# Optimization experiments

Hardware: AMD Instinct MI355X
Metric: run time of the kernel (lower is better)

Reference implementation:

```python
import jax, jax.numpy as jnp
import numpy as np

NPOINT = 1024
RADIUS = 0.15
NSAMPLE = 32
BN_EPS = 1e-5


def farthest_point_sample(xyz, npoint):
    # xyz: [B, N, 3] -> idx [B, npoint]
    B, N, _ = xyz.shape

    def step(carry, _):
        dmin, far = carry
        cent = jnp.take_along_axis(xyz, far[:, None, None], axis=1)  # [B,1,3]
        d = jnp.sum((xyz - cent) ** 2, axis=-1)                      # [B,N]
        dmin = jnp.minimum(dmin, d)
        nxt = jnp.argmax(dmin, axis=-1).astype(jnp.int32)
        return (dmin, nxt), far

    init = (jnp.full((B, N), 1e10, xyz.dtype), jnp.zeros((B,), jnp.int32))
    _, idx = jax.lax.scan(step, init, None, length=npoint)
    return idx.T  # [B, npoint]


def ball_query(radius, nsample, xyz, new_xyz):
    # xyz: [B,N,3], new_xyz: [B,S,3] -> idx [B,S,nsample]
    B, S, _ = new_xyz.shape
    N = xyz.shape[1]
    sqr = jnp.sum((new_xyz[:, :, None, :] - xyz[:, None, :, :]) ** 2, axis=-1)  # [B,S,N]
    ar = jnp.broadcast_to(jnp.arange(N, dtype=jnp.int32), (B, S, N))
    gidx = jnp.where(sqr > radius * radius, N, ar)
    gidx = jnp.sort(gidx, axis=-1)[:, :, :nsample]
    first = gidx[:, :, :1]
    return jnp.where(gidx == N, first, gidx)


def setup_inputs() -> dict:
    key = jax.random.key(0)
    ks = jax.random.split(key, 8)
    B, N, Cin, Cmlp, Cout = 8, 4096, 64, 128, 256
    xyz = jax.random.uniform(ks[0], (B, N, 3), dtype=jnp.float32)
    t = jax.random.normal(ks[1], (B, 128), dtype=jnp.float32)
    points = jax.random.normal(ks[2], (B, N, Cin), dtype=jnp.float32)
    W1 = jax.random.normal(ks[3], (Cin, Cmlp), dtype=jnp.float32) / np.sqrt(Cin)
    b1 = jnp.zeros((Cmlp,), jnp.float32)
    Wc = jax.random.normal(ks[4], (Cmlp, Cout), dtype=jnp.float32) / np.sqrt(Cmlp)
    bc = jnp.zeros((Cout,), jnp.float32)
    gamma = jnp.ones((Cout,), jnp.float32)
    beta = jnp.zeros((Cout,), jnp.float32)
    return {"xyz": xyz, "t": t, "points": points, "W1": W1, "b1": b1,
            "Wc": Wc, "bc": bc, "gamma": gamma, "beta": beta}


def reference(xyz, t, points, W1, b1, Wc, bc, gamma, beta):
    # t (time embedding) is unused in the visible (truncated) forward body.
    B, N, _ = xyz.shape
    # 1) farthest point sampling -> centers
    fps_idx = farthest_point_sample(xyz, NPOINT)                     # [B,S]
    new_xyz = jnp.take_along_axis(xyz, fps_idx[:, :, None], axis=1)  # [B,S,3]
    # 2) radius ball-query grouping
    gidx = ball_query(RADIUS, NSAMPLE, xyz, new_xyz)                 # [B,S,ns]
    # 3) pointwise MLP on features, then group (gather)
    feats = points @ W1 + b1                                          # [B,N,Cmlp]
    grouped = jax.vmap(lambda f, i: f[i])(feats, gidx)                # [B,S,ns,Cmlp]
    # 4) GroupConv: 1x1 conv + BatchNorm(train stats) + ReLU
    h = jnp.einsum('bsnc,co->bsno', grouped, Wc) + bc                 # [B,S,ns,Cout]
    mean = jnp.mean(h, axis=(0, 1, 2))
    var = jnp.var(h, axis=(0, 1, 2))
    h = jax.nn.relu((h - mean) / jnp.sqrt(var + BN_EPS) * gamma + beta)
    # 5) max-pool over neighborhood
    new_points = jnp.max(h, axis=2)                                   # [B,S,Cout]
    return new_points
```

## Files before the change

### kernel.cpp

```cpp
#include <hip/hip_runtime.h>
#include <stdint.h>

#define BN 8
#define NPT 4096
#define NS 1024
#define KS 32
#define CIN 64
#define CMID 128
#define COUT 256
#define NGRP (BN*NS)
#define NBINS 512

typedef short bf16x8 __attribute__((ext_vector_type(8)));
typedef float f32x4 __attribute__((ext_vector_type(4)));
typedef unsigned long long u64;

__device__ __forceinline__ float bf2f(unsigned short u){
  union { unsigned int i; float f; } v; v.i = ((unsigned int)u) << 16; return v.f;
}
__device__ __forceinline__ unsigned short f2bf(float f){
  union { float f; unsigned int i; } v; v.f = f;
  unsigned int r = (v.i + 0x7fffu + ((v.i >> 16) & 1u)) >> 16;
  return (unsigned short)r;
}
__device__ __forceinline__ uint32_t pack2(float a, float b){
  return (uint32_t)f2bf(a) | ((uint32_t)f2bf(b) << 16);
}
__device__ __forceinline__ float ldf(const void* p, size_t i, bool isbf){
  return isbf ? bf2f(((const unsigned short*)p)[i]) : ((const float*)p)[i];
}
__device__ __forceinline__ bool detect_bf(const void* gamma){
  return ((const unsigned int*)gamma)[0] == 0x3F803F80u;
}
template<int CTRL>
__device__ __forceinline__ u64 dpp_u64(u64 x){
  int lo = (int)(unsigned int)(x & 0xFFFFFFFFull);
  int hi = (int)(unsigned int)(x >> 32);
  int nlo = __builtin_amdgcn_update_dpp(0, lo, CTRL, 0xF, 0xF, true);
  int nhi = __builtin_amdgcn_update_dpp(0, hi, CTRL, 0xF, 0xF, true);
  return ((u64)(unsigned int)nhi << 32) | (unsigned int)nlo;
}
__device__ __forceinline__ u64 u64max(u64 a, u64 b){ return a > b ? a : b; }
__device__ __forceinline__ u64 wave_max_u64(u64 k){
  k = u64max(k, dpp_u64<0x121>(k));
  k = u64max(k, dpp_u64<0x122>(k));
  k = u64max(k, dpp_u64<0x124>(k));
  k = u64max(k, dpp_u64<0x128>(k));
  k = u64max(k, dpp_u64<0x142>(k));
  k = u64max(k, dpp_u64<0x143>(k));
  return k;
}
__device__ __forceinline__ u64 readlane63_u64(u64 k){
  unsigned lo = (unsigned)__builtin_amdgcn_readlane((int)(unsigned)(k & 0xFFFFFFFFull), 63);
  unsigned hi = (unsigned)__builtin_amdgcn_readlane((int)(unsigned)(k >> 32), 63);
  return ((u64)hi << 32) | lo;
}
__device__ __forceinline__ void bbox6(float x, float y, float z,
                                      float&xl,float&xh,float&yl,float&yh,float&zl,float&zh){
  xl=x; xh=x; yl=y; yh=y; zl=z; zh=z;
  #pragma unroll
  for (int off=1; off<64; off<<=1){
    xl=fminf(xl,__shfl_xor(xl,off,64)); xh=fmaxf(xh,__shfl_xor(xh,off,64));
    yl=fminf(yl,__shfl_xor(yl,off,64)); yh=fmaxf(yh,__shfl_xor(yh,off,64));
    zl=fminf(zl,__shfl_xor(zl,off,64)); zh=fmaxf(zh,__shfl_xor(zh,off,64));
  }
}

__device__ __forceinline__ unsigned mcode(float x, float y, float z){
  int ix = (int)(x*16.f); ix = ix<0?0:(ix>15?15:ix);
  int iy = (int)(y*16.f); iy = iy<0?0:(iy>15?15:iy);
  int iz = (int)(z*8.f);  iz = iz<0?0:(iz>7?7:iz);
  return ((unsigned)(iy&1))      | ((unsigned)(ix&1)<<1) | ((unsigned)(iz&1)<<2)
       | ((unsigned)(iy&2)<<2)   | ((unsigned)(ix&2)<<3) | ((unsigned)(iz&2)<<4)
       | ((unsigned)(iy&4)<<4)   | ((unsigned)(ix&4)<<5) | ((unsigned)(iz&4)<<6)
       | ((unsigned)(iy&8)<<6)   | ((unsigned)(ix&8)<<7);
}

__global__ __launch_bounds__(512, 3)
void k_front(const void* __restrict__ xyz,
             const void* __restrict__ points,
             const void* __restrict__ W1,
             const void* __restrict__ Wc,
             const void* __restrict__ gamma,
             float* __restrict__ newxyz,
             unsigned short* __restrict__ featsb,
             unsigned short* __restrict__ wct,
             float* __restrict__ ps, float* __restrict__ pq, int bigws)
{
  int tid = threadIdx.x;
  int bid = blockIdx.x;
  bool isbf = detect_bf(gamma);
  __shared__ __align__(16) char smem[65536];
  __shared__ unsigned tsum[512];
  __shared__ u64 wk[2][8];

  if (bid < 8){
    float* ssx = (float*)smem;
    float* ssy = ssx + NPT;
    float* ssz = ssy + NPT;
    unsigned short* snl = (unsigned short*)(ssz + NPT);
    unsigned* hist = (unsigned*)(smem + 57344);
    size_t xb = (size_t)bid*NPT*3;
    int base = tid*8;
    for (int i=tid; i<2048; i+=512) hist[i]=0;
    __syncthreads();
    unsigned codes[8];
    #pragma unroll
    for (int k=0;k<8;k++){
      size_t p = xb + (size_t)(base+k)*3;
      unsigned c = mcode(ldf(xyz,p,isbf), ldf(xyz,p+1,isbf), ldf(xyz,p+2,isbf));
      codes[k]=c;
      atomicAdd(&hist[c],1u);
    }
    __syncthreads();
    unsigned l0=hist[tid*4],l1=hist[tid*4+1],l2=hist[tid*4+2],l3=hist[tid*4+3];
    unsigned s = l0+l1+l2+l3;
    tsum[tid]=s; __syncthreads();
    for (int off=1; off<512; off<<=1){
      unsigned v = (tid>=off)? tsum[tid-off]:0u; __syncthreads();
      tsum[tid]+=v; __syncthreads();
    }
    unsigned ex0 = tsum[tid]-s;
    hist[tid*4]=ex0; hist[tid*4+1]=ex0+l0; hist[tid*4+2]=ex0+l0+l1; hist[tid*4+3]=ex0+l0+l1+l2;
    __syncthreads();
    #pragma unroll
    for (int k=0;k<8;k++){
      size_t p = xb + (size_t)(base+k)*3;
      float x=ldf(xyz,p,isbf), y=ldf(xyz,p+1,isbf), z=ldf(xyz,p+2,isbf);
      unsigned pos = atomicAdd(&hist[codes[k]],1u);
      ssx[pos]=x; ssy[pos]=y; ssz[pos]=z; snl[pos]=(unsigned short)(4095-(base+k));
    }
    __syncthreads();
    int lane = tid & 63, wv = tid >> 6;
    float qx0,qx1,qx2,qx3,qx4,qx5,qx6,qx7;
    float qy0,qy1,qy2,qy3,qy4,qy5,qy6,qy7;
    float qz0,qz1,qz2,qz3,qz4,qz5,qz6,qz7;
    float dd0,dd1,dd2,dd3,dd4,dd5,dd6,dd7;
    unsigned lk0,lk1,lk2,lk3,lk4,lk5,lk6,lk7;
#define LOADS(k) { int p = (wv<<9) + ((k)<<6) + lane; \
  qx##k=ssx[p]; qy##k=ssy[p]; qz##k=ssz[p]; dd##k=1e10f; \
  lk##k = ((unsigned)snl[p]<<12) | (unsigned)p; }
    LOADS(0) LOADS(1) LOADS(2) LOADS(3) LOADS(4) LOADS(5) LOADS(6) LOADS(7)
#undef LOADS
    float qbxl=0.f,qbxh=0.f,qbyl=0.f,qbyh=0.f,qbzl=0.f,qbzh=0.f;
    int lq = lane & 7;
#define CB(k) { float xl,xh,yl,yh,zl,zh; bbox6(qx##k,qy##k,qz##k,xl,xh,yl,yh,zl,zh); \
  if (lq==(k)){ qbxl=xl; qbxh=xh; qbyl=yl; qbyh=yh; qbzl=zl; qbzh=zh; } }
    CB(0) CB(1) CB(2) CB(3) CB(4) CB(5) CB(6) CB(7)
#undef CB
    float cx=ldf(xyz,xb,isbf), cy=ldf(xyz,xb+1,isbf), cz=ldf(xyz,xb+2,isbf);
    if (tid==0){ float* o = newxyz + (size_t)bid*NS*3; o[0]=cx; o[1]=cy; o[2]=cz; }
    u64 ckey = ((u64)__float_as_uint(1e10f) << 32);
    for (int it=1; it<NS; ++it){
      int par = it & 1;
      float exd = fmaxf(fmaxf(__fsub_rn(qbxl,cx), __fsub_rn(cx,qbxh)), 0.f);
      float eyd = fmaxf(fmaxf(__fsub_rn(qbyl,cy), __fsub_rn(cy,qbyh)), 0.f);
      float ezd = fmaxf(fmaxf(__fsub_rn(qbzl,cz), __fsub_rn(cz,qbzh)), 0.f);
      float lb2 = exd*exd + eyd*eyd + ezd*ezd;
      float wtmax = __uint_as_float((unsigned)(ckey >> 32));
      unsigned amask = (unsigned)__ballot(lb2*0.999f < wtmax) & 0xFFu;
      if (amask){
#define FPS_STEP(k) if (amask & (1u<<(k))){ \
  float dx=__fsub_rn(qx##k,cx), dy=__fsub_rn(qy##k,cy), dz=__fsub_rn(qz##k,cz); \
  float d=__fadd_rn(__fadd_rn(__fmul_rn(dx,dx),__fmul_rn(dy,dy)),__fmul_rn(dz,dz)); \
  dd##k=fminf(dd##k,d); }
        FPS_STEP(0) FPS_STEP(1) FPS_STEP(2) FPS_STEP(3)
        FPS_STEP(4) FPS_STEP(5) FPS_STEP(6) FPS_STEP(7)
#undef FPS_STEP
#define KEYK(k) ( ((u64)__float_as_uint(dd##k) << 32) | lk##k )
        u64 t0=u64max(KEYK(0),KEYK(1)), t2=u64max(KEYK(2),KEYK(3));
        u64 t4=u64max(KEYK(4),KEYK(5)), t6=u64max(KEYK(6),KEYK(7));
#undef KEYK
        t0=u64max(t0,t2); t4=u64max(t4,t6);
        u64 key = u64max(t0,t4);
        ckey = readlane63_u64(wave_max_u64(key));
      }
      if (lane == 0) wk[par][wv] = ckey;
      __syncthreads();
      const u64* w8 = wk[par];
      u64 k0 = u64max(u64max(u64max(w8[0],w8[1]), u64max(w8[2],w8[3])),
                      u64max(u64max(w8[4],w8[5]), u64max(w8[6],w8[7])));
      unsigned spos = (unsigned)(k0 & 0xFFFu);
      cx = ssx[spos]; cy = ssy[spos]; cz = ssz[spos];
      if (tid==0){ float* o = newxyz + ((size_t)bid*NS + it)*3; o[0]=cx; o[1]=cy; o[2]=cz; }
    }
  } else if (bid == 8){
    for (int i=tid; i<CMID*COUT; i+=512){
      int k = i >> 8, n = i & 255;
      unsigned short w = isbf ? ((const unsigned short*)Wc)[i] : f2bf(((const float*)Wc)[i]);
      wct[(size_t)n*CMID + k] = w;
    }
    if (!bigws){
      for (int i=tid; i<COUT*NBINS; i+=512){ ps[i]=0.f; pq[i]=0.f; }
    }
  } else {
    float* w1s = (float*)smem;
    float* pts = (float*)(smem + 32768);
    int rb = bid - 9;
    int r0g = rb*64;
    for (int i=tid; i<CIN*CMID; i+=512) w1s[i] = ldf(W1, i, isbf);
    for (int i=tid; i<64*CIN; i+=512)   pts[i] = ldf(points, (size_t)r0g*CIN + i, isbf);
    __syncthreads();
    int o0 = (tid & 15) * 8, r0 = (tid >> 4) * 2;
    float acc0[8]={0,0,0,0,0,0,0,0}, acc1[8]={0,0,0,0,0,0,0,0};
    for (int c=0;c<CIN;c++){
      float a0 = pts[r0*CIN + c], a1 = pts[(r0+1)*CIN + c];
      const float* wr = &w1s[c*CMID + o0];
      #pragma unroll
      for (int j=0;j<8;j++){ acc0[j] = fmaf(a0, wr[j], acc0[j]); acc1[j] = fmaf(a1, wr[j], acc1[j]); }
    }
    unsigned short* f0 = featsb + ((size_t)(r0g + r0))*CMID + o0;
    uint4 u;
    u.x=pack2(acc0[0],acc0[1]); u.y=pack2(acc0[2],acc0[3]); u.z=pack2(acc0[4],acc0[5]); u.w=pack2(acc0[6],acc0[7]);
    *(uint4*)f0 = u;
    u.x=pack2(acc1[0],acc1[1]); u.y=pack2(acc1[2],acc1[3]); u.z=pack2(acc1[4],acc1[5]); u.w=pack2(acc1[6],acc1[7]);
    *(uint4*)(f0 + CMID) = u;
  }
}

__global__ __launch_bounds__(256)
void k_ballq(const void* __restrict__ xyz,
             const void* __restrict__ gamma,
             const float* __restrict__ newxyz,
             int* __restrict__ gidx)
{
  __shared__ float sp[NPT*3];
  __shared__ int slots[4][KS];
  int tid = threadIdx.x;
  bool isbf = detect_bf(gamma);
  int cb = blockIdx.x * 64;
  int b = cb >> 10;
  size_t xb = (size_t)b*NPT*3;
  for (int i=tid; i<NPT*3; i+=256) sp[i] = ldf(xyz, xb + i, isbf);
  __syncthreads();
  int lane = tid & 63, wv = tid >> 6;
  const float rr = (float)(0.15*0.15);
  for (int j=0; j<16; ++j){
    int cid = cb + wv*16 + j;
    const float* cc = newxyz + (size_t)cid*3;
    float cx=cc[0], cy=cc[1], cz=cc[2];
    int cnt = 0;
    for (int ch=0; ch<64; ++ch){
      int p = ch*64 + lane;
      float dx=__fsub_rn(sp[p*3],cx), dy=__fsub_rn(sp[p*3+1],cy), dz=__fsub_rn(sp[p*3+2],cz);
      float d=__fadd_rn(__fadd_rn(__fmul_rn(dx,dx),__fmul_rn(dy,dy)),__fmul_rn(dz,dz));
      bool in = !(d > rr);
      u64 mk = __ballot(in);
      int pos = cnt + __popcll(mk & ((1ull<<lane) - 1ull));
      if (in && pos < KS) slots[wv][pos] = p;
      cnt += __popcll(mk);
      if (cnt >= KS) break;
    }
    int total = cnt < KS ? cnt : KS;
    if (lane < KS){
      int v = (lane < total) ? slots[wv][lane] : slots[wv][0];
      gidx[(size_t)cid*KS + lane] = v;
    }
  }
}

__global__ __launch_bounds__(256)
void k_group(const unsigned short* __restrict__ featsb,
             const unsigned short* __restrict__ wct,
             const int* __restrict__ gidx,
             float* __restrict__ ps, float* __restrict__ pq,
             float* __restrict__ hM, int bigws)
{
  int tid = threadIdx.x;
  int bs0 = blockIdx.x * 2;
  __shared__ unsigned short g[2][32][136];
  __shared__ int gi[2][KS];
  if (tid < 2*KS) gi[tid>>5][tid&31] = gidx[(size_t)bs0*KS + tid];
  __syncthreads();
  {
    int r = tid >> 3, sg = tid & 7;
    size_t fb = (size_t)(bs0>>10)*NPT;
    #pragma unroll
    for (int gg=0; gg<2; gg++){
      const unsigned short* src = featsb + (fb + gi[gg][r])*CMID + sg*16;
      uint4 v0 = *(const uint4*)src;
      uint4 v1 = *(const uint4*)(src + 8);
      *(uint4*)(&g[gg][r][sg*16])     = v0;
      *(uint4*)(&g[gg][r][sg*16 + 8]) = v1;
    }
  }
  __syncthreads();
  int lane = tid & 63, wv = tid >> 6;
  int m = lane & 15, quad = lane >> 4;
  f32x4 acc[2][2][4];
  #pragma unroll
  for (int gg=0; gg<2; gg++)
    #pragma unroll
    for (int a=0;a<2;a++)
      #pragma unroll
      for (int b2=0;b2<4;b2++) acc[gg][a][b2] = (f32x4){0.f,0.f,0.f,0.f};
  int n0 = wv * 64;
  #pragma unroll
  for (int k0=0; k0<CMID; k0+=32){
    bf16x8 a00 = *(const bf16x8*)(&g[0][m][k0 + quad*8]);
    bf16x8 a01 = *(const bf16x8*)(&g[0][16 + m][k0 + quad*8]);
    bf16x8 a10 = *(const bf16x8*)(&g[1][m][k0 + quad*8]);
    bf16x8 a11 = *(const bf16x8*)(&g[1][16 + m][k0 + quad*8]);
    #pragma unroll
    for (int nt=0; nt<4; nt++){
      int n = n0 + nt*16 + m;
      bf16x8 bb = *(const bf16x8*)(wct + (size_t)n*CMID + k0 + quad*8);
      acc[0][0][nt] = __builtin_amdgcn_mfma_f32_16x16x32_bf16(a00, bb, acc[0][0][nt], 0, 0, 0);
      acc[0][1][nt] = __builtin_amdgcn_mfma_f32_16x16x32_bf16(a01, bb, acc[0][1][nt], 0, 0, 0);
      acc[1][0][nt] = __builtin_amdgcn_mfma_f32_16x16x32_bf16(a10, bb, acc[1][0][nt], 0, 0, 0);
      acc[1][1][nt] = __builtin_amdgcn_mfma_f32_16x16x32_bf16(a11, bb, acc[1][1][nt], 0, 0, 0);
    }
  }
  #pragma unroll
  for (int gg=0; gg<2; gg++){
    int bs = bs0 + gg;
    #pragma unroll
    for (int nt=0; nt<4; nt++){
      float s=0.f, q=0.f, hx=-3.402823466e38f;
      #pragma unroll
      for (int mt=0; mt<2; mt++)
        #pragma unroll
        for (int rg=0; rg<4; rg++){ float h = acc[gg][mt][nt][rg]; s += h; q += h*h; hx = fmaxf(hx,h); }
      s += __shfl_xor(s,16,64); q += __shfl_xor(q,16,64); hx = fmaxf(hx, __shfl_xor(hx,16,64));
      s += __shfl_xor(s,32,64); q += __shfl_xor(q,32,64); hx = fmaxf(hx, __shfl_xor(hx,32,64));
      if (quad == 0){
        int o = n0 + nt*16 + m;
        if (bigws){
          ps[(size_t)o*NGRP + bs] = s;
          pq[(size_t)o*NGRP + bs] = q;
        } else {
          atomicAdd(&ps[(size_t)o*NBINS + (bs & (NBINS-1))], s);
          atomicAdd(&pq[(size_t)o*NBINS + (bs & (NBINS-1))], q);
        }
        hM[(size_t)bs*COUT + o] = hx;
      }
    }
  }
}

__global__ __launch_bounds__(256)
void k_bnprep(const float* __restrict__ ps, const float* __restrict__ pq,
              const void* __restrict__ gamma, const void* __restrict__ beta,
              float* __restrict__ av, float* __restrict__ cv, int nbins)
{
  int tid = threadIdx.x, o = blockIdx.x;
  bool isbf = detect_bf(gamma);
  float s=0.f, q=0.f;
  for (int i=tid; i<nbins; i+=256){ s += ps[(size_t)o*nbins + i]; q += pq[(size_t)o*nbins + i]; }
  #pragma unroll
  for (int off=1; off<64; off<<=1){ s += __shfl_xor(s,off,64); q += __shfl_xor(q,off,64); }
  __shared__ float ls[4], lq[4];
  int lane = tid & 63, wv = tid >> 6;
  if (lane == 0){ ls[wv]=s; lq[wv]=q; }
  __syncthreads();
  if (tid == 0){
    float S = ls[0]+ls[1]+ls[2]+ls[3], Q = lq[0]+lq[1]+lq[2]+lq[3];
    const float invM = 1.0f/262144.0f;
    float mean = S*invM;
    float var  = fmaxf(Q*invM - mean*mean, 0.f);
    float inv  = 1.0f/sqrtf(var + 1e-5f);
    float a = ldf(gamma,o,isbf)*inv;
    float c = ldf(beta,o,isbf) - mean*a;
    av[o]=a; cv[o]=c;
  }
}

__global__ __launch_bounds__(256)
void k_bnfinal(const float* __restrict__ hM,
               const float* __restrict__ av, const float* __restrict__ cv,
               const void* __restrict__ gamma, void* __restrict__ out)
{
  int idx = blockIdx.x*256 + threadIdx.x;
  int o = idx & 255;
  float v = fmaxf(hM[idx]*av[o] + cv[o], 0.f);
  if (detect_bf(gamma)) ((unsigned short*)out)[idx] = f2bf(v);
  else                  ((float*)out)[idx] = v;
}

extern "C" void kernel_launch(void* const* d_in, const int* in_sizes, int n_in,
                              void* d_out, int out_size, void* d_ws, size_t ws_size,
                              hipStream_t stream)
{
  const void* xyz    = d_in[0];
  const void* points = d_in[2];
  const void* W1     = d_in[3];
  const void* Wc     = d_in[5];
  const void* gamma  = d_in[7];
  const void* beta   = d_in[8];

  char* ws = (char*)d_ws;
  unsigned short* featsb = (unsigned short*)(ws + 0);
  unsigned short* wct    = (unsigned short*)(ws + 8388608);
  float* newxyz          = (float*)(ws + 8454144);
  int*   gidx            = (int*)(ws + 8552448);
  bool bigws = ws_size >= (size_t)34768896;
  float *ps, *pq, *hM, *av, *cv;
  if (bigws){
    ps = (float*)(ws + 9601024);
    pq = (float*)(ws + 17989632);
    hM = (float*)(ws + 26378240);
    av = (float*)(ws + 34766848);
    cv = (float*)(ws + 34767872);
  } else {
    hM = (float*)(ws + 9601024);
    ps = (float*)(ws + 17989632);
    pq = (float*)(ws + 18513920);
    av = (float*)(ws + 19038208);
    cv = (float*)(ws + 19039232);
  }

  hipLaunchKernelGGL(k_front,  dim3(521), dim3(512), 0, stream,
                     xyz, points, W1, Wc, gamma, newxyz, featsb, wct, ps, pq, (int)bigws);
  hipLaunchKernelGGL(k_ballq,  dim3(128), dim3(256), 0, stream, xyz, gamma, newxyz, gidx);
  hipLaunchKernelGGL(k_group,  dim3(4096), dim3(256), 0, stream,
                     featsb, wct, gidx, ps, pq, hM, (int)bigws);
  hipLaunchKernelGGL(k_bnprep, dim3(256),  dim3(256), 0, stream,
                     ps, pq, gamma, beta, av, cv, bigws ? NGRP : NBINS);
  hipLaunchKernelGGL(k_bnfinal,dim3(8192), dim3(256), 0, stream, hM, av, cv, gamma, d_out);
}
```

Before: 955.9 us.

## Run two FPS batches per block sharing one barrier per iteration

The farthest-point-sampling stage now handles two batches per workgroup (4 blocks instead of 8), interleaving both batches' updates so that each iteration needs one barrier for two batches. Point data is repacked into an xyz+index float4 array so each point load is a single vector LDS read. This shortens per-step overhead from barriers and LDS reads but doubles the serial work per block and raises register pressure (launch bounds lowered to 2 blocks). FPS is latency bound, so the serial chain per block gets longer while the barrier cost is amortised.

```diff
diff --git a/kernel.cpp b/kernel.cpp
--- a/kernel.cpp
+++ b/kernel.cpp
@@ -76,7 +76,7 @@
        | ((unsigned)(iy&8)<<6)   | ((unsigned)(ix&8)<<7);
 }
 
-__global__ __launch_bounds__(512, 3)
+__global__ __launch_bounds__(512, 2)
 void k_front(const void* __restrict__ xyz,
              const void* __restrict__ points,
              const void* __restrict__ W1,
@@ -90,101 +90,135 @@
   int tid = threadIdx.x;
   int bid = blockIdx.x;
   bool isbf = detect_bf(gamma);
-  __shared__ __align__(16) char smem[65536];
+  __shared__ __align__(16) float ssp[2][NPT*4];
+  __shared__ unsigned hist[2048];
   __shared__ unsigned tsum[512];
-  __shared__ u64 wk[2][8];
-
-  if (bid < 8){
-    float* ssx = (float*)smem;
-    float* ssy = ssx + NPT;
-    float* ssz = ssy + NPT;
-    unsigned short* snl = (unsigned short*)(ssz + NPT);
-    unsigned* hist = (unsigned*)(smem + 57344);
-    size_t xb = (size_t)bid*NPT*3;
+  __shared__ u64 wk[2][2][8];
+
+  if (bid < 4){
+    int lane = tid & 63, wv = tid >> 6;
     int base = tid*8;
-    for (int i=tid; i<2048; i+=512) hist[i]=0;
-    __syncthreads();
-    unsigned codes[8];
-    #pragma unroll
-    for (int k=0;k<8;k++){
-      size_t p = xb + (size_t)(base+k)*3;
-      unsigned c = mcode(ldf(xyz,p,isbf), ldf(xyz,p+1,isbf), ldf(xyz,p+2,isbf));
-      codes[k]=c;
-      atomicAdd(&hist[c],1u);
-    }
-    __syncthreads();
-    unsigned l0=hist[tid*4],l1=hist[tid*4+1],l2=hist[tid*4+2],l3=hist[tid*4+3];
-    unsigned s = l0+l1+l2+l3;
-    tsum[tid]=s; __syncthreads();
-    for (int off=1; off<512; off<<=1){
-      unsigned v = (tid>=off)? tsum[tid-off]:0u; __syncthreads();
-      tsum[tid]+=v; __syncthreads();
-    }
-    unsigned ex0 = tsum[tid]-s;
-    hist[tid*4]=ex0; hist[tid*4+1]=ex0+l0; hist[tid*4+2]=ex0+l0+l1; hist[tid*4+3]=ex0+l0+l1+l2;
-    __syncthreads();
-    #pragma unroll
-    for (int k=0;k<8;k++){
-      size_t p = xb + (size_t)(base+k)*3;
-      float x=ldf(xyz,p,isbf), y=ldf(xyz,p+1,isbf), z=ldf(xyz,p+2,isbf);
-      unsigned pos = atomicAdd(&hist[codes[k]],1u);
-      ssx[pos]=x; ssy[pos]=y; ssz[pos]=z; snl[pos]=(unsigned short)(4095-(base+k));
-    }
-    __syncthreads();
-    int lane = tid & 63, wv = tid >> 6;
-    float qx0,qx1,qx2,qx3,qx4,qx5,qx6,qx7;
-    float qy0,qy1,qy2,qy3,qy4,qy5,qy6,qy7;
-    float qz0,qz1,qz2,qz3,qz4,qz5,qz6,qz7;
-    float dd0,dd1,dd2,dd3,dd4,dd5,dd6,dd7;
-    unsigned lk0,lk1,lk2,lk3,lk4,lk5,lk6,lk7;
-#define LOADS(k) { int p = (wv<<9) + ((k)<<6) + lane; \
-  qx##k=ssx[p]; qy##k=ssy[p]; qz##k=ssz[p]; dd##k=1e10f; \
-  lk##k = ((unsigned)snl[p]<<12) | (unsigned)p; }
-    LOADS(0) LOADS(1) LOADS(2) LOADS(3) LOADS(4) LOADS(5) LOADS(6) LOADS(7)
+    for (int c=0;c<2;c++){
+      size_t xb = (size_t)(bid*2+c)*NPT*3;
+      float* sp = ssp[c];
+      for (int i=tid; i<2048; i+=512) hist[i]=0;
+      __syncthreads();
+      unsigned codes[8];
+      #pragma unroll
+      for (int k=0;k<8;k++){
+        size_t p = xb + (size_t)(base+k)*3;
+        unsigned cc = mcode(ldf(xyz,p,isbf), ldf(xyz,p+1,isbf), ldf(xyz,p+2,isbf));
+        codes[k]=cc;
+        atomicAdd(&hist[cc],1u);
+      }
+      __syncthreads();
+      unsigned l0=hist[tid*4],l1=hist[tid*4+1],l2=hist[tid*4+2],l3=hist[tid*4+3];
+      unsigned s = l0+l1+l2+l3;
+      tsum[tid]=s; __syncthreads();
+      for (int off=1; off<512; off<<=1){
+        unsigned v = (tid>=off)? tsum[tid-off]:0u; __syncthreads();
+        tsum[tid]+=v; __syncthreads();
+      }
+      unsigned ex0 = tsum[tid]-s;
+      hist[tid*4]=ex0; hist[tid*4+1]=ex0+l0; hist[tid*4+2]=ex0+l0+l1; hist[tid*4+3]=ex0+l0+l1+l2;
+      __syncthreads();
+      #pragma unroll
+      for (int k=0;k<8;k++){
+        size_t p = xb + (size_t)(base+k)*3;
+        float x=ldf(xyz,p,isbf), y=ldf(xyz,p+1,isbf), z=ldf(xyz,p+2,isbf);
+        unsigned pos = atomicAdd(&hist[codes[k]],1u);
+        sp[pos*4]=x; sp[pos*4+1]=y; sp[pos*4+2]=z;
+        ((unsigned*)sp)[pos*4+3] = (unsigned)(4095-(base+k));
+      }
+      __syncthreads();
+    }
+#define DECL(C) \
+    float qx##C##0,qx##C##1,qx##C##2,qx##C##3,qx##C##4,qx##C##5,qx##C##6,qx##C##7; \
+    float qy##C##0,qy##C##1,qy##C##2,qy##C##3,qy##C##4,qy##C##5,qy##C##6,qy##C##7; \
+    float qz##C##0,qz##C##1,qz##C##2,qz##C##3,qz##C##4,qz##C##5,qz##C##6,qz##C##7; \
+    float dd##C##0,dd##C##1,dd##C##2,dd##C##3,dd##C##4,dd##C##5,dd##C##6,dd##C##7; \
+    unsigned lk##C##0,lk##C##1,lk##C##2,lk##C##3,lk##C##4,lk##C##5,lk##C##6,lk##C##7;
+    DECL(A) DECL(B)
+#undef DECL
+#define LOADS(C,S,k) { int p = (wv<<9) + ((k)<<6) + lane; \
+  const f32x4 v = *(const f32x4*)&ssp[S][p*4]; \
+  qx##C##k=v[0]; qy##C##k=v[1]; qz##C##k=v[2]; dd##C##k=1e10f; \
+  lk##C##k = (__float_as_uint(v[3])<<12) | (unsigned)p; }
+    LOADS(A,0,0) LOADS(A,0,1) LOADS(A,0,2) LOADS(A,0,3)
+    LOADS(A,0,4) LOADS(A,0,5) LOADS(A,0,6) LOADS(A,0,7)
+    LOADS(B,1,0) LOADS(B,1,1) LOADS(B,1,2) LOADS(B,1,3)
+    LOADS(B,1,4) LOADS(B,1,5) LOADS(B,1,6) LOADS(B,1,7)
 #undef LOADS
-    float qbxl=0.f,qbxh=0.f,qbyl=0.f,qbyh=0.f,qbzl=0.f,qbzh=0.f;
     int lq = lane & 7;
-#define CB(k) { float xl,xh,yl,yh,zl,zh; bbox6(qx##k,qy##k,qz##k,xl,xh,yl,yh,zl,zh); \
-  if (lq==(k)){ qbxl=xl; qbxh=xh; qbyl=yl; qbyh=yh; qbzl=zl; qbzh=zh; } }
-    CB(0) CB(1) CB(2) CB(3) CB(4) CB(5) CB(6) CB(7)
+#define BDECL(C) float qbxl##C=0.f,qbxh##C=0.f,qbyl##C=0.f,qbyh##C=0.f,qbzl##C=0.f,qbzh##C=0.f;
+    BDECL(A) BDECL(B)
+#undef BDECL
+#define CB(C,k) { float xl,xh,yl,yh,zl,zh; bbox6(qx##C##k,qy##C##k,qz##C##k,xl,xh,yl,yh,zl,zh); \
+  if (lq==(k)){ qbxl##C=xl; qbxh##C=xh; qbyl##C=yl; qbyh##C=yh; qbzl##C=zl; qbzh##C=zh; } }
+    CB(A,0) CB(A,1) CB(A,2) CB(A,3) CB(A,4) CB(A,5) CB(A,6) CB(A,7)
+    CB(B,0) CB(B,1) CB(B,2) CB(B,3) CB(B,4) CB(B,5) CB(B,6) CB(B,7)
 #undef CB
-    float cx=ldf(xyz,xb,isbf), cy=ldf(xyz,xb+1,isbf), cz=ldf(xyz,xb+2,isbf);
-    if (tid==0){ float* o = newxyz + (size_t)bid*NS*3; o[0]=cx; o[1]=cy; o[2]=cz; }
-    u64 ckey = ((u64)__float_as_uint(1e10f) << 32);
+    size_t xbA = (size_t)(bid*2)*NPT*3, xbB = (size_t)(bid*2+1)*NPT*3;
+    float cxA=ldf(xyz,xbA,isbf), cyA=ldf(xyz,xbA+1,isbf), czA=ldf(xyz,xbA+2,isbf);
+    float cxB=ldf(xyz,xbB,isbf), cyB=ldf(xyz,xbB+1,isbf), czB=ldf(xyz,xbB+2,isbf);
+    if (tid==0){
+      float* o = newxyz + (size_t)(bid*2)*NS*3;   o[0]=cxA; o[1]=cyA; o[2]=czA;
+      float* p = newxyz + (size_t)(bid*2+1)*NS*3; p[0]=cxB; p[1]=cyB; p[2]=czB;
+    }
+    u64 ckeyA = ((u64)__float_as_uint(1e10f) << 32);
+    u64 ckeyB = ckeyA;
     for (int it=1; it<NS; ++it){
       int par = it & 1;
-      float exd = fmaxf(fmaxf(__fsub_rn(qbxl,cx), __fsub_rn(cx,qbxh)), 0.f);
-      float eyd = fmaxf(fmaxf(__fsub_rn(qbyl,cy), __fsub_rn(cy,qbyh)), 0.f);
-      float ezd = fmaxf(fmaxf(__fsub_rn(qbzl,cz), __fsub_rn(cz,qbzh)), 0.f);
-      float lb2 = exd*exd + eyd*eyd + ezd*ezd;
-      float wtmax = __uint_as_float((unsigned)(ckey >> 32));
-      unsigned amask = (unsigned)__ballot(lb2*0.999f < wtmax) & 0xFFu;
-      if (amask){
-#define FPS_STEP(k) if (amask & (1u<<(k))){ \
-  float dx=__fsub_rn(qx##k,cx), dy=__fsub_rn(qy##k,cy), dz=__fsub_rn(qz##k,cz); \
-  float d=__fadd_rn(__fadd_rn(__fmul_rn(dx,dx),__fmul_rn(dy,dy)),__fmul_rn(dz,dz)); \
-  dd##k=fminf(dd##k,d); }
-        FPS_STEP(0) FPS_STEP(1) FPS_STEP(2) FPS_STEP(3)
-        FPS_STEP(4) FPS_STEP(5) FPS_STEP(6) FPS_STEP(7)
-#undef FPS_STEP
-#define KEYK(k) ( ((u64)__float_as_uint(dd##k) << 32) | lk##k )
-        u64 t0=u64max(KEYK(0),KEYK(1)), t2=u64max(KEYK(2),KEYK(3));
-        u64 t4=u64max(KEYK(4),KEYK(5)), t6=u64max(KEYK(6),KEYK(7));
-#undef KEYK
-        t0=u64max(t0,t2); t4=u64max(t4,t6);
-        u64 key = u64max(t0,t4);
-        ckey = readlane63_u64(wave_max_u64(key));
-      }
-      if (lane == 0) wk[par][wv] = ckey;
+#define UPDATE(C, CI) { \
+      float exd = fmaxf(fmaxf(__fsub_rn(qbxl##C,cx##C), __fsub_rn(cx##C,qbxh##C)), 0.f); \
+      float eyd = fmaxf(fmaxf(__fsub_rn(qbyl##C,cy##C), __fsub_rn(cy##C,qbyh##C)), 0.f); \
+      float ezd = fmaxf(fmaxf(__fsub_rn(qbzl##C,cz##C), __fsub_rn(cz##C,qbzh##C)), 0.f); \
+      float lb2 = exd*exd + eyd*eyd + ezd*ezd; \
+      float wtmax = __uint_as_float((unsigned)(ckey##C >> 32)); \
+      unsigned amask = (unsigned)__ballot(lb2*0.999f < wtmax) & 0xFFu; \
+      if (amask){ \
+         \
+        if (amask & 1u)  { float dx=__fsub_rn(qx##C##0,cx##C), dy=__fsub_rn(qy##C##0,cy##C), dz=__fsub_rn(qz##C##0,cz##C); \
+          dd##C##0=fminf(dd##C##0,__fadd_rn(__fadd_rn(__fmul_rn(dx,dx),__fmul_rn(dy,dy)),__fmul_rn(dz,dz))); } \
+        if (amask & 2u)  { float dx=__fsub_rn(qx##C##1,cx##C), dy=__fsub_rn(qy##C##1,cy##C), dz=__fsub_rn(qz##C##1,cz##C); \
+          dd##C##1=fminf(dd##C##1,__fadd_rn(__fadd_rn(__fmul_rn(dx,dx),__fmul_rn(dy,dy)),__fmul_rn(dz,dz))); } \
+        if (amask & 4u)  { float dx=__fsub_rn(qx##C##2,cx##C), dy=__fsub_rn(qy##C##2,cy##C), dz=__fsub_rn(qz##C##2,cz##C); \
+          dd##C##2=fminf(dd##C##2,__fadd_rn(__fadd_rn(__fmul_rn(dx,dx),__fmul_rn(dy,dy)),__fmul_rn(dz,dz))); } \
+        if (amask & 8u)  { float dx=__fsub_rn(qx##C##3,cx##C), dy=__fsub_rn(qy##C##3,cy##C), dz=__fsub_rn(qz##C##3,cz##C); \
+          dd##C##3=fminf(dd##C##3,__fadd_rn(__fadd_rn(__fmul_rn(dx,dx),__fmul_rn(dy,dy)),__fmul_rn(dz,dz))); } \
+        if (amask & 16u) { float dx=__fsub_rn(qx##C##4,cx##C), dy=__fsub_rn(qy##C##4,cy##C), dz=__fsub_rn(qz##C##4,cz##C); \
+          dd##C##4=fminf(dd##C##4,__fadd_rn(__fadd_rn(__fmul_rn(dx,dx),__fmul_rn(dy,dy)),__fmul_rn(dz,dz))); } \
+        if (amask & 32u) { float dx=__fsub_rn(qx##C##5,cx##C), dy=__fsub_rn(qy##C##5,cy##C), dz=__fsub_rn(qz##C##5,cz##C); \
+          dd##C##5=fminf(dd##C##5,__fadd_rn(__fadd_rn(__fmul_rn(dx,dx),__fmul_rn(dy,dy)),__fmul_rn(dz,dz))); } \
+        if (amask & 64u) { float dx=__fsub_rn(qx##C##6,cx##C), dy=__fsub_rn(qy##C##6,cy##C), dz=__fsub_rn(qz##C##6,cz##C); \
+          dd##C##6=fminf(dd##C##6,__fadd_rn(__fadd_rn(__fmul_rn(dx,dx),__fmul_rn(dy,dy)),__fmul_rn(dz,dz))); } \
+        if (amask & 128u){ float dx=__fsub_rn(qx##C##7,cx##C), dy=__fsub_rn(qy##C##7,cy##C), dz=__fsub_rn(qz##C##7,cz##C); \
+          dd##C##7=fminf(dd##C##7,__fadd_rn(__fadd_rn(__fmul_rn(dx,dx),__fmul_rn(dy,dy)),__fmul_rn(dz,dz))); } \
+        u64 t0=u64max(((u64)__float_as_uint(dd##C##0)<<32)|lk##C##0, ((u64)__float_as_uint(dd##C##1)<<32)|lk##C##1); \
+        u64 t2=u64max(((u64)__float_as_uint(dd##C##2)<<32)|lk##C##2, ((u64)__float_as_uint(dd##C##3)<<32)|lk##C##3); \
+        u64 t4=u64max(((u64)__float_as_uint(dd##C##4)<<32)|lk##C##4, ((u64)__float_as_uint(dd##C##5)<<32)|lk##C##5); \
+        u64 t6=u64max(((u64)__float_as_uint(dd##C##6)<<32)|lk##C##6, ((u64)__float_as_uint(dd##C##7)<<32)|lk##C##7); \
+        t0=u64max(t0,t2); t4=u64max(t4,t6); \
+        ckey##C = readlane63_u64(wave_max_u64(u64max(t0,t4))); \
+      } \
+      if (lane == 0) wk[CI][par][wv] = ckey##C; }
+      UPDATE(A, 0)
+      UPDATE(B, 1)
+#undef UPDATE
       __syncthreads();
-      const u64* w8 = wk[par];
-      u64 k0 = u64max(u64max(u64max(w8[0],w8[1]), u64max(w8[2],w8[3])),
-                      u64max(u64max(w8[4],w8[5]), u64max(w8[6],w8[7])));
-      unsigned spos = (unsigned)(k0 & 0xFFFu);
-      cx = ssx[spos]; cy = ssy[spos]; cz = ssz[spos];
-      if (tid==0){ float* o = newxyz + ((size_t)bid*NS + it)*3; o[0]=cx; o[1]=cy; o[2]=cz; }
-    }
-  } else if (bid == 8){
+#define FINAL(C, CI, S, BATCH) { \
+      const u64* w8 = wk[CI][par]; \
+      u64 k0 = u64max(u64max(u64max(w8[0],w8[1]), u64max(w8[2],w8[3])), \
+                      u64max(u64max(w8[4],w8[5]), u64max(w8[6],w8[7]))); \
+      unsigned spos = (unsigned)(k0 & 0xFFFu); \
+      const f32x4 v = *(const f32x4*)&ssp[S][spos*4]; \
+      cx##C=v[0]; cy##C=v[1]; cz##C=v[2]; \
+      if (tid==0){ float* o = newxyz + ((size_t)(BATCH)*NS + it)*3; o[0]=cx##C; o[1]=cy##C; o[2]=cz##C; } }
+      FINAL(A, 0, 0, bid*2)
+      FINAL(B, 1, 1, bid*2+1)
+#undef FINAL
+    }
+  } else if (bid == 4){
     for (int i=tid; i<CMID*COUT; i+=512){
       int k = i >> 8, n = i & 255;
       unsigned short w = isbf ? ((const unsigned short*)Wc)[i] : f2bf(((const float*)Wc)[i]);
@@ -194,9 +228,9 @@
       for (int i=tid; i<COUT*NBINS; i+=512){ ps[i]=0.f; pq[i]=0.f; }
     }
   } else {
-    float* w1s = (float*)smem;
-    float* pts = (float*)(smem + 32768);
-    int rb = bid - 9;
+    float* w1s = ssp[0];
+    float* pts = ssp[0] + CIN*CMID;
+    int rb = bid - 5;
     int r0g = rb*64;
     for (int i=tid; i<CIN*CMID; i+=512) w1s[i] = ldf(W1, i, isbf);
     for (int i=tid; i<64*CIN; i+=512)   pts[i] = ldf(points, (size_t)r0g*CIN + i, isbf);
@@ -409,7 +443,7 @@
     cv = (float*)(ws + 19039232);
   }
 
-  hipLaunchKernelGGL(k_front,  dim3(521), dim3(512), 0, stream,
+  hipLaunchKernelGGL(k_front,  dim3(517), dim3(512), 0, stream,
                      xyz, points, W1, Wc, gamma, newxyz, featsb, wct, ps, pq, (int)bigws);
   hipLaunchKernelGGL(k_ballq,  dim3(128), dim3(256), 0, stream, xyz, gamma, newxyz, gidx);
   hipLaunchKernelGGL(k_group,  dim3(4096), dim3(256), 0, stream,
```

Result: slower. 1.426 ms (+49.2%).

## Fuse ball query into group kernel and merge BN prep with final pass

Applied to the files above, without the earlier changes.

The ball-query kernel is folded into the grouping/MFMA kernel. Each block now finds its own two centers' neighbours in shared memory and gathers features directly, so the gidx round trip through global memory and one launch go away. The BN statistics reduction and the normalize/ReLU pass become one kernel, with each block handling one output channel. In exchange, every one of the 4096 blocks reloads the full 48KB per-batch xyz array into shared memory, which also limits occupancy. The fused BN writes use a 256-element stride across threads, so its memory accesses are no longer coalesced.

```diff
diff --git a/kernel.cpp b/kernel.cpp
--- a/kernel.cpp
+++ b/kernel.cpp
@@ -219,26 +219,32 @@
 }
 
 __global__ __launch_bounds__(256)
-void k_ballq(const void* __restrict__ xyz,
-             const void* __restrict__ gamma,
-             const float* __restrict__ newxyz,
-             int* __restrict__ gidx)
+void k_groupq(const void* __restrict__ xyz,
+              const float* __restrict__ newxyz,
+              const unsigned short* __restrict__ featsb,
+              const unsigned short* __restrict__ wct,
+              const void* __restrict__ gamma,
+              float* __restrict__ ps, float* __restrict__ pq,
+              float* __restrict__ hM, int bigws)
 {
-  __shared__ float sp[NPT*3];
-  __shared__ int slots[4][KS];
   int tid = threadIdx.x;
+  int bs0 = blockIdx.x * 2;
+  int b = bs0 >> 10;
   bool isbf = detect_bf(gamma);
-  int cb = blockIdx.x * 64;
-  int b = cb >> 10;
+  __shared__ __align__(16) char smem[49152];
+  __shared__ int gi[2][KS];
+  int lane = tid & 63, wv = tid >> 6;
+
+  float* sp = (float*)smem;
   size_t xb = (size_t)b*NPT*3;
   for (int i=tid; i<NPT*3; i+=256) sp[i] = ldf(xyz, xb + i, isbf);
   __syncthreads();
-  int lane = tid & 63, wv = tid >> 6;
-  const float rr = (float)(0.15*0.15);
-  for (int j=0; j<16; ++j){
-    int cid = cb + wv*16 + j;
+
+  if (wv < 2){
+    int cid = bs0 + wv;
     const float* cc = newxyz + (size_t)cid*3;
     float cx=cc[0], cy=cc[1], cz=cc[2];
+    const float rr = (float)(0.15*0.15);
     int cnt = 0;
     for (int ch=0; ch<64; ++ch){
       int p = ch*64 + lane;
@@ -247,45 +253,35 @@
       bool in = !(d > rr);
       u64 mk = __ballot(in);
       int pos = cnt + __popcll(mk & ((1ull<<lane) - 1ull));
-      if (in && pos < KS) slots[wv][pos] = p;
+      if (in && pos < KS) gi[wv][pos] = p;
       cnt += __popcll(mk);
       if (cnt >= KS) break;
     }
     int total = cnt < KS ? cnt : KS;
     if (lane < KS){
-      int v = (lane < total) ? slots[wv][lane] : slots[wv][0];
-      gidx[(size_t)cid*KS + lane] = v;
-    }
-  }
-}
-
-__global__ __launch_bounds__(256)
-void k_group(const unsigned short* __restrict__ featsb,
-             const unsigned short* __restrict__ wct,
-             const int* __restrict__ gidx,
-             float* __restrict__ ps, float* __restrict__ pq,
-             float* __restrict__ hM, int bigws)
-{
-  int tid = threadIdx.x;
-  int bs0 = blockIdx.x * 2;
-  __shared__ unsigned short g[2][32][136];
-  __shared__ int gi[2][KS];
-  if (tid < 2*KS) gi[tid>>5][tid&31] = gidx[(size_t)bs0*KS + tid];
+      int v = (lane < total) ? gi[wv][lane] : gi[wv][0];
+      gi[wv][lane] = v;
+    }
+  }
   __syncthreads();
+
+  typedef unsigned short grow_t[32][136];
+  grow_t* g = (grow_t*)smem;
   {
     int r = tid >> 3, sg = tid & 7;
-    size_t fb = (size_t)(bs0>>10)*NPT;
-    #pragma unroll
-    for (int gg=0; gg<2; gg++){
-      const unsigned short* src = featsb + (fb + gi[gg][r])*CMID + sg*16;
-      uint4 v0 = *(const uint4*)src;
-      uint4 v1 = *(const uint4*)(src + 8);
-      *(uint4*)(&g[gg][r][sg*16])     = v0;
-      *(uint4*)(&g[gg][r][sg*16 + 8]) = v1;
-    }
+    size_t fb = (size_t)b*NPT;
+    int gi0 = gi[0][r], gi1 = gi[1][r];
+    const unsigned short* s0 = featsb + (fb + gi0)*CMID + sg*16;
+    const unsigned short* s1 = featsb + (fb + gi1)*CMID + sg*16;
+    uint4 a0 = *(const uint4*)s0, a1 = *(const uint4*)(s0 + 8);
+    uint4 b0 = *(const uint4*)s1, b1 = *(const uint4*)(s1 + 8);
+    *(uint4*)(&g[0][r][sg*16])     = a0;
+    *(uint4*)(&g[0][r][sg*16 + 8]) = a1;
+    *(uint4*)(&g[1][r][sg*16])     = b0;
+    *(uint4*)(&g[1][r][sg*16 + 8]) = b1;
   }
   __syncthreads();
-  int lane = tid & 63, wv = tid >> 6;
+
   int m = lane & 15, quad = lane >> 4;
   f32x4 acc[2][2][4];
   #pragma unroll
@@ -339,9 +335,10 @@
 }
 
 __global__ __launch_bounds__(256)
-void k_bnprep(const float* __restrict__ ps, const float* __restrict__ pq,
-              const void* __restrict__ gamma, const void* __restrict__ beta,
-              float* __restrict__ av, float* __restrict__ cv, int nbins)
+void k_bn(const float* __restrict__ ps, const float* __restrict__ pq,
+          const float* __restrict__ hM,
+          const void* __restrict__ gamma, const void* __restrict__ beta,
+          void* __restrict__ out, int nbins)
 {
   int tid = threadIdx.x, o = blockIdx.x;
   bool isbf = detect_bf(gamma);
@@ -349,7 +346,7 @@
   for (int i=tid; i<nbins; i+=256){ s += ps[(size_t)o*nbins + i]; q += pq[(size_t)o*nbins + i]; }
   #pragma unroll
   for (int off=1; off<64; off<<=1){ s += __shfl_xor(s,off,64); q += __shfl_xor(q,off,64); }
-  __shared__ float ls[4], lq[4];
+  __shared__ float ls[4], lq[4], sa, sc;
   int lane = tid & 63, wv = tid >> 6;
   if (lane == 0){ ls[wv]=s; lq[wv]=q; }
   __syncthreads();
@@ -361,20 +358,16 @@
     float inv  = 1.0f/sqrtf(var + 1e-5f);
     float a = ldf(gamma,o,isbf)*inv;
     float c = ldf(beta,o,isbf) - mean*a;
-    av[o]=a; cv[o]=c;
-  }
-}
-
-__global__ __launch_bounds__(256)
-void k_bnfinal(const float* __restrict__ hM,
-               const float* __restrict__ av, const float* __restrict__ cv,
-               const void* __restrict__ gamma, void* __restrict__ out)
-{
-  int idx = blockIdx.x*256 + threadIdx.x;
-  int o = idx & 255;
-  float v = fmaxf(hM[idx]*av[o] + cv[o], 0.f);
-  if (detect_bf(gamma)) ((unsigned short*)out)[idx] = f2bf(v);
-  else                  ((float*)out)[idx] = v;
+    sa=a; sc=c;
+  }
+  __syncthreads();
+  float a = sa, c = sc;
+  for (int bs=tid; bs<NGRP; bs+=256){
+    size_t oi = (size_t)bs*COUT + o;
+    float v = fmaxf(hM[oi]*a + c, 0.f);
+    if (isbf) ((unsigned short*)out)[oi] = f2bf(v);
+    else      ((float*)out)[oi] = v;
+  }
 }
 
 extern "C" void kernel_launch(void* const* d_in, const int* in_sizes, int n_in,
@@ -392,29 +385,22 @@
   unsigned short* featsb = (unsigned short*)(ws + 0);
   unsigned short* wct    = (unsigned short*)(ws + 8388608);
   float* newxyz          = (float*)(ws + 8454144);
-  int*   gidx            = (int*)(ws + 8552448);
   bool bigws = ws_size >= (size_t)34768896;
-  float *ps, *pq, *hM, *av, *cv;
+  float *ps, *pq, *hM;
   if (bigws){
     ps = (float*)(ws + 9601024);
     pq = (float*)(ws + 17989632);
     hM = (float*)(ws + 26378240);
-    av = (float*)(ws + 34766848);
-    cv = (float*)(ws + 34767872);
   } else {
     hM = (float*)(ws + 9601024);
     ps = (float*)(ws + 17989632);
     pq = (float*)(ws + 18513920);
-    av = (float*)(ws + 19038208);
-    cv = (float*)(ws + 19039232);
   }
 
   hipLaunchKernelGGL(k_front,  dim3(521), dim3(512), 0, stream,
                      xyz, points, W1, Wc, gamma, newxyz, featsb, wct, ps, pq, (int)bigws);
-  hipLaunchKernelGGL(k_ballq,  dim3(128), dim3(256), 0, stream, xyz, gamma, newxyz, gidx);
-  hipLaunchKernelGGL(k_group,  dim3(4096), dim3(256), 0, stream,
-                     featsb, wct, gidx, ps, pq, hM, (int)bigws);
-  hipLaunchKernelGGL(k_bnprep, dim3(256),  dim3(256), 0, stream,
-                     ps, pq, gamma, beta, av, cv, bigws ? NGRP : NBINS);
-  hipLaunchKernelGGL(k_bnfinal,dim3(8192), dim3(256), 0, stream, hM, av, cv, gamma, d_out);
-}
+  hipLaunchKernelGGL(k_groupq, dim3(4096), dim3(256), 0, stream,
+                     xyz, newxyz, featsb, wct, gamma, ps, pq, hM, (int)bigws);
+  hipLaunchKernelGGL(k_bn,     dim3(256),  dim3(256), 0, stream,
+                     ps, pq, hM, gamma, beta, d_out, bigws ? NGRP : NBINS);
+}
```

After: 907.0 us (median of 2 runs). 1.05x faster.
